# Kernel optimization log

Measured on AMD Instinct MI355X. Metric: run time of the kernel, lower is better.

Reference implementation:

```python
import jax, jax.numpy as jnp
import numpy as np

N, D, K = 65536, 256, 4096
INIT_COUNT = 100  # torch: counts = ones(K, int32) * 100


def setup_inputs() -> dict:
    key = jax.random.key(0)
    k1, k2 = jax.random.split(key)
    embedded = jax.random.normal(k1, (N, D), dtype=jnp.float32)
    centers = jax.random.normal(k2, (K, D), dtype=jnp.float32)
    counts = jnp.full((K,), INIT_COUNT, dtype=jnp.int32)
    return {"embedded": embedded, "centers": centers, "counts": counts}


def reference(embedded, centers, counts):
    # --- predict_hard: squared euclidean distance [N,K] + argmin ---
    x2 = jnp.sum(embedded * embedded, axis=1, keepdims=True)       # [N,1]
    c2 = jnp.sum(centers * centers, axis=1)                        # [K]
    d2 = x2 - 2.0 * (embedded @ centers.T) + c2                    # [N,K]
    labels = jnp.argmin(d2, axis=1).astype(jnp.int32)              # [N]

    # --- dcn_loss: mean over batch of squared dist to assigned center ---
    loss = jnp.sum((embedded - centers[labels]) ** 2) / embedded.shape[0]

    # --- update_centroids: sequential running-mean update, closed form ---
    # c <- (1-1/n)c + (1/n)x repeated over assigned samples collapses to
    # (count0 * c0 + sum_assigned x) / (count0 + m)
    seg_sum = jax.ops.segment_sum(embedded, labels, num_segments=K)            # [K,D]
    seg_cnt = jax.ops.segment_sum(
        jnp.ones((embedded.shape[0],), dtype=embedded.dtype), labels, num_segments=K
    )                                                                           # [K]
    c0 = counts.astype(embedded.dtype)                                          # [K]
    new_centers = (c0[:, None] * centers + seg_sum) / (c0 + seg_cnt)[:, None]  # [K,D]
    new_counts = counts + seg_cnt.astype(jnp.int32)                             # [K]
    return labels, new_centers, new_counts, loss
```

## Files before the change

### kernel.cpp

```cpp
#include <hip/hip_runtime.h>
#include <cfloat>
#include <cstdint>

constexpr int N  = 65536;
constexpr int D  = 256;
constexpr int K  = 4096;

typedef __attribute__((ext_vector_type(8))) _Float16 half8;
typedef __attribute__((ext_vector_type(8))) unsigned short ushort8;
typedef __attribute__((ext_vector_type(4))) float floatx4;

__device__ __forceinline__ floatx4 mfma_f16(half8 a, half8 b, floatx4 c) {
    return __builtin_amdgcn_mfma_f32_16x16x32_f16(a, b, c, 0, 0, 0);
}

__device__ __forceinline__ void ld_lds16(void* lds, const void* g) {
    __builtin_amdgcn_global_load_lds(
        (const __attribute__((address_space(1))) unsigned int*)g,
        (__attribute__((address_space(3))) unsigned int*)lds, 16, 0, 0);
}

__global__ void prep_c2(const float* __restrict__ C, float* __restrict__ c2) {
    int k = blockIdx.x;
    int l = threadIdx.x;
    const float4* row = (const float4*)(C + (size_t)k * D);
    float4 v = row[l];
    float s = v.x*v.x + v.y*v.y + v.z*v.z + v.w*v.w;
    #pragma unroll
    for (int m = 1; m < 64; m <<= 1) s += __shfl_xor(s, m);
    if (l == 0) c2[k] = s;
}

__global__ void convert_f16_both(const float* __restrict__ X, const float* __restrict__ C,
                                 unsigned short* __restrict__ Xh,
                                 unsigned short* __restrict__ Cf,
                                 float* __restrict__ xsq_part,
                                 float* __restrict__ c2) {
    __shared__ float red[4];
    int id = blockIdx.x * 256 + threadIdx.x;
    const int nX = N * D / 8;
    bool isX = id < nX;
    const float* src;
    if (isX) { src = X; }
    else     { src = C; id -= nX; }
    const float4* s4 = (const float4*)src;
    float4 a = s4[2*id], b = s4[2*id+1];
    float xs[8] = {a.x,a.y,a.z,a.w,b.x,b.y,b.z,b.w};
    ushort8 h;
    float ps = 0.f;
    #pragma unroll
    for (int i = 0; i < 8; ++i) {
        union { _Float16 f; unsigned short u; } cv;
        cv.f = (_Float16)xs[i];
        h[i] = cv.u;
        ps += xs[i]*xs[i];
    }
    int t = threadIdx.x;
    if (isX) {
        ((ushort8*)Xh)[id] = h;
        #pragma unroll
        for (int m = 1; m < 64; m <<= 1) ps += __shfl_xor(ps, m);
        if ((t & 63) == 0) red[t >> 6] = ps;
        __syncthreads();
        if (t == 0) xsq_part[blockIdx.x] = (red[0] + red[1]) + (red[2] + red[3]);
    } else {
        int c    = id >> 5;
        int dk   = (id >> 2) & 7;
        int quad = id & 3;
        int flat = (((c >> 6) * 8 + dk) * 4 + ((c >> 4) & 3)) * 64 + quad * 16 + (c & 15);
        ((ushort8*)Cf)[flat] = h;
        #pragma unroll
        for (int m = 1; m < 32; m <<= 1) ps += __shfl_xor(ps, m);
        if ((t & 31) == 0) c2[c] = ps;
    }
}

__global__ __launch_bounds__(256, 2) void mfma_assign(
        const unsigned short* __restrict__ Xh, const unsigned short* __restrict__ Cfu,
        const float* __restrict__ c2, float* __restrict__ cand)
{
    __shared__ __align__(16) unsigned short sA[8*128*4*8];

    const int t    = threadIdx.x;
    const int w    = t >> 6, l = t & 63;
    const int quad = l >> 4, lr = l & 15;
    const int wm   = w >> 1, wn = w & 1;
    const int rowbase = blockIdx.x * 128;
    const int kb   = blockIdx.y;

    const int rl  = l >> 2;
    const int gsw = (l & 3) ^ ((l >> 3) & 3);

    #pragma unroll
    for (int k = 0; k < 16; ++k) {
        int q = w*16 + k;
        int c = q >> 3, rb = (q & 7) * 16;
        const unsigned short* gp = Xh + (size_t)(rowbase + rb + rl)*D + c*32 + gsw*8;
        ld_lds16((char*)sA + q*1024, gp);
    }

    const half8* pB = (const half8*)Cfu + (size_t)(kb*16 + wn)*2048 + l;
    const char* sAc = (const char*)sA;
    const int sA_off = ((64*wm + lr)*4 + (quad ^ ((lr>>1)&3)))*16;

    half8 A0[4], A1[4], B0[4], B1[4];

#define LOADB(Bs, bump) do {                                            \
        Bs[0] = pB[0]; Bs[1] = pB[64]; Bs[2] = pB[128]; Bs[3] = pB[192]; \
        pB += (bump); } while (0)

#define LOADA(As, dkn) do {                                             \
        As[0] = *(const half8*)(sAc + ((dkn)*8192 + 0*1024) + sA_off);  \
        As[1] = *(const half8*)(sAc + ((dkn)*8192 + 1*1024) + sA_off);  \
        As[2] = *(const half8*)(sAc + ((dkn)*8192 + 2*1024) + sA_off);  \
        As[3] = *(const half8*)(sAc + ((dkn)*8192 + 3*1024) + sA_off); } while (0)

#define MF16(As, Bs) do {                                               \
        _Pragma("unroll")                                               \
        for (int j_ = 0; j_ < 4; ++j_)                                  \
            _Pragma("unroll")                                           \
            for (int i_ = 0; i_ < 4; ++i_)                              \
                acc[i_][j_] = mfma_f16(As[i_], Bs[j_], acc[i_][j_]); } while (0)

    LOADB(B0, 256);
    __syncthreads();
    LOADA(A0, 0);

    float v1[16], v2[16]; int x1[16], x2s[16];
    #pragma unroll
    for (int i = 0; i < 16; ++i) { v1[i]=FLT_MAX; v2[i]=FLT_MAX; x1[i]=0x7fffffff; x2s[i]=0x7fffffff; }

    floatx4 acc[4][4];
    float c2v[4]; int jidx[4];

    for (int e = 0; e < 8; ++e) {
        #pragma unroll
        for (int i = 0; i < 4; ++i)
            #pragma unroll
            for (int j = 0; j < 4; ++j) acc[i][j] = (floatx4)0.f;
        const int colbase = (kb*8 + e)*128 + 64*wn;
        #pragma unroll
        for (int j = 0; j < 4; ++j) {
            int col = colbase + 16*j + lr;
            c2v[j] = c2[col]; jidx[j] = col;
        }

        LOADB(B1, 256);  LOADA(A1, 1); MF16(A0, B0);
        LOADB(B0, 256);  LOADA(A0, 2); MF16(A1, B1);
        LOADB(B1, 256);  LOADA(A1, 3); MF16(A0, B0);
        LOADB(B0, 256);  LOADA(A0, 4); MF16(A1, B1);
        LOADB(B1, 256);  LOADA(A1, 5); MF16(A0, B0);
        LOADB(B0, 256);  LOADA(A0, 6); MF16(A1, B1);
        LOADB(B1, 2304); LOADA(A1, 7); MF16(A0, B0);
        LOADB(B0, 256);  LOADA(A0, 0); MF16(A1, B1);

        #pragma unroll
        for (int i = 0; i < 4; ++i)
            #pragma unroll
            for (int j = 0; j < 4; ++j)
                #pragma unroll
                for (int r = 0; r < 4; ++r) {
                    float s = fmaf(-2.f, acc[i][j][r], c2v[j]);
                    int st = 4*i + r;
                    bool cA = s < v1[st];
                    bool cB = s < v2[st];
                    float tv = cB ? s : v2[st]; int tx = cB ? jidx[j] : x2s[st];
                    v2[st] = cA ? v1[st] : tv;  x2s[st] = cA ? x1[st] : tx;
                    v1[st] = cA ? s : v1[st];   x1[st]  = cA ? jidx[j] : x1[st];
                }
    }

#undef LOADB
#undef LOADA
#undef MF16

    #pragma unroll
    for (int i = 0; i < 4; ++i)
        #pragma unroll
        for (int r = 0; r < 4; ++r) {
            int st = 4*i + r;
            float a1 = v1[st], a2 = v2[st]; int ax1 = x1[st], ax2 = x2s[st];
            #pragma unroll
            for (int m = 1; m < 16; m <<= 1) {
                float b1f = __shfl_xor(a1, m); int bx1 = __shfl_xor(ax1, m);
                float b2f = __shfl_xor(a2, m); int bx2 = __shfl_xor(ax2, m);
                bool tt = (b1f < a1) || (b1f == a1 && bx1 < ax1);
                float n1 = tt ? b1f : a1; int nx1 = tt ? bx1 : ax1;
                float w1 = tt ? a1 : b1f; int wx1 = tt ? ax1 : bx1;
                float w2 = tt ? b2f : a2; int wx2 = tt ? bx2 : ax2;
                bool uu = (w2 < w1) || (w2 == w1 && wx2 < wx1);
                a1 = n1; ax1 = nx1;
                a2 = uu ? w2 : w1; ax2 = uu ? wx2 : wx1;
            }
            if (lr == 0) {
                int row = rowbase + 64*wm + 16*i + 4*quad + r;
                float4 o; o.x = a1; o.y = __int_as_float(ax1);
                o.z = a2; o.w = __int_as_float(ax2);
                ((float4*)cand)[(size_t)row*8 + 2*kb + wn] = o;
            }
        }
}

__global__ __launch_bounds__(256) void recheck_label(
        const float* __restrict__ X, const float* __restrict__ C,
        const float* __restrict__ c2, const float* __restrict__ cand,
        float* __restrict__ out_labels, int* __restrict__ labInt,
        int* __restrict__ cnt)
{
    int t = threadIdx.x, w = t >> 6, l = t & 63;
    int g  = l >> 4;
    int lr = l & 15;
    int row0 = (blockIdx.x * 4 + w) * 4;
    int row  = row0 + g;

    float4 e = ((const float4*)cand)[(size_t)row*8 + (lr >> 1)];
    float s  = (lr & 1) ? e.z : e.x;
    int  idx = (lr & 1) ? __float_as_int(e.w) : __float_as_int(e.y);

    float a1 = s, a2 = FLT_MAX; int ax1 = idx, ax2 = 0x7fffffff;
    #pragma unroll
    for (int m = 1; m < 16; m <<= 1) {
        float b1 = __shfl_xor(a1, m); int bx1 = __shfl_xor(ax1, m);
        float b2 = __shfl_xor(a2, m); int bx2 = __shfl_xor(ax2, m);
        bool tt = (b1 < a1) || (b1 == a1 && bx1 < ax1);
        float n1 = tt ? b1 : a1; int nx1 = tt ? bx1 : ax1;
        float w1 = tt ? a1 : b1; int wx1 = tt ? ax1 : bx1;
        float w2 = tt ? b2 : a2; int wx2 = tt ? bx2 : ax2;
        bool uu = (w2 < w1) || (w2 == w1 && wx2 < wx1);
        a1 = n1; ax1 = nx1;
        a2 = uu ? w2 : w1; ax2 = uu ? wx2 : wx1;
    }

    bool certain = (a2 - a1 > 0.25f);
    unsigned long long certMask = __ballot(certain);

    if (certain && lr == 0) {
        out_labels[row] = (float)ax1;
        labInt[row] = ax1;
        atomicAdd(&cnt[ax1], 1);
    }

    #pragma unroll
    for (int q = 0; q < 4; ++q) {
        if ((certMask >> (q*16)) & 1ull) continue;
        int r = row0 + q;
        float sq  = __shfl(s,   q*16 + lr);
        int   iq  = __shfl(idx, q*16 + lr);
        float gs1 = __shfl(a1,  q*16);

        float4 xv = ((const float4*)X)[(size_t)r*64 + l];
        float px = xv.x*xv.x + xv.y*xv.y + xv.z*xv.z + xv.w*xv.w;
        #pragma unroll
        for (int m = 1; m < 64; m <<= 1) px += __shfl_xor(px, m);

        bool active = (l < 16) && (sq <= gs1 + 0.25f);
        unsigned long long mask = __ballot(active);
        float best = FLT_MAX; int bi = 0x7fffffff;
        while (mask) {
            int k = __ffsll((long long)mask) - 1;
            mask &= mask - 1;
            int ck = __shfl(iq, k);
            float4 cv = ((const float4*)C)[(size_t)ck*64 + l];
            float pd = xv.x*cv.x + xv.y*cv.y + xv.z*cv.z + xv.w*cv.w;
            #pragma unroll
            for (int m = 1; m < 64; m <<= 1) pd += __shfl_xor(pd, m);
            float d2 = fmaf(-2.f, pd, px) + c2[ck];
            if (d2 < best || (d2 == best && ck < bi)) { best = d2; bi = ck; }
        }
        if (l == 0) {
            out_labels[r] = (float)bi;
            labInt[r] = bi;
            atomicAdd(&cnt[bi], 1);
        }
    }
}

__global__ void prefix_kernel(const int* __restrict__ cnt,
                              int* __restrict__ offs, int* __restrict__ cursor) {
    int l = threadIdx.x;
    int s = 0;
    #pragma unroll 8
    for (int i = 0; i < 64; ++i) s += cnt[l*64 + i];
    int inc = s;
    #pragma unroll
    for (int off = 1; off < 64; off <<= 1) {
        int u = __shfl_up(inc, off);
        if (l >= off) inc += u;
    }
    int run = inc - s;
    for (int i = 0; i < 64; ++i) {
        int k = l*64 + i;
        offs[k] = run; cursor[k] = run;
        run += cnt[k];
    }
}

__global__ void scatter_idx(const int* __restrict__ labInt,
                            int* __restrict__ cursor, int* __restrict__ sortedIdx) {
    int i = blockIdx.x * 256 + threadIdx.x;
    int lab = labInt[i];
    int pos = atomicAdd(&cursor[lab], 1);
    sortedIdx[pos] = i;
}

__global__ __launch_bounds__(256) void center_update(
        const float* __restrict__ X, const float* __restrict__ C,
        const int* __restrict__ counts0, const int* __restrict__ cnt,
        const int* __restrict__ offs, const int* __restrict__ sortedIdx,
        float* __restrict__ lossC, float* __restrict__ out)
{
    __shared__ float red[4];
    int k = blockIdx.x, d = threadIdx.x;
    int start = offs[k], m = cnt[k];
    float acc = 0.f;
    int i = 0;
    for (; i + 4 <= m; i += 4) {
        int r0 = sortedIdx[start+i],   r1 = sortedIdx[start+i+1];
        int r2 = sortedIdx[start+i+2], r3 = sortedIdx[start+i+3];
        float a0 = X[(size_t)r0*D + d], a1 = X[(size_t)r1*D + d];
        float a2 = X[(size_t)r2*D + d], a3 = X[(size_t)r3*D + d];
        acc += (a0 + a1) + (a2 + a3);
    }
    for (; i < m; ++i) acc += X[(size_t)sortedIdx[start+i]*D + d];

    float cv = C[(size_t)k*D + d];
    float c0 = (float)counts0[k];
    out[N + (size_t)k*D + d] = (c0 * cv + acc) / (c0 + (float)m);
    if (d == 0) out[N + (size_t)K*D + k] = (float)(counts0[k] + m);

    float lp = cv * fmaf((float)m, cv, -2.f*acc);
    #pragma unroll
    for (int s = 1; s < 64; s <<= 1) lp += __shfl_xor(lp, s);
    if ((d & 63) == 0) red[d >> 6] = lp;
    __syncthreads();
    if (d == 0) lossC[k] = (red[0] + red[1]) + (red[2] + red[3]);
}

__global__ __launch_bounds__(256) void loss_final(
        const float* __restrict__ xsq_part, const float* __restrict__ lossC,
        float* __restrict__ out)
{
    __shared__ double red[4];
    int t = threadIdx.x;
    double s = 0.0;
    for (int i = t; i < 8192; i += 256) s += (double)xsq_part[i];
    for (int i = t; i < 4096; i += 256) s += (double)lossC[i];
    #pragma unroll
    for (int m = 1; m < 64; m <<= 1) s += __shfl_xor(s, m);
    if ((t & 63) == 0) red[t >> 6] = s;
    __syncthreads();
    if (t == 0)
        out[N + (size_t)K*D + K] = (float)(((red[0] + red[1]) + (red[2] + red[3])) / (double)N);
}

__global__ void finalize_kernel(const float* __restrict__ C,
                                const int* __restrict__ counts0,
                                const float* __restrict__ seg,
                                const int* __restrict__ cnt,
                                const double* __restrict__ lossAcc,
                                float* __restrict__ out)
{
    int g = blockIdx.x * 256 + threadIdx.x;
    int k = g >> 8;
    float c0 = (float)counts0[k];
    float m  = (float)cnt[k];
    out[N + g] = (c0 * C[g] + seg[g]) / (c0 + m);
    if (g < K) out[N + (size_t)K*D + g] = (float)(counts0[g] + cnt[g]);
    if (g == 0) out[N + (size_t)K*D + K] = (float)(lossAcc[0] / (double)N);
}

__global__ __launch_bounds__(256, 2) void assign_fp32(
        const float* __restrict__ X, const float* __restrict__ C,
        const float* __restrict__ c2, float* __restrict__ out_labels,
        float* __restrict__ seg, int* __restrict__ cnt,
        double* __restrict__ lossAcc)
{
    constexpr int BM = 128, BN = 128, KD = 16;
    __shared__ float As[KD][BM];
    __shared__ float Bs[KD][BN];
    __shared__ float x2f[BM];
    __shared__ int   labs[BM];

    const int t  = threadIdx.x;
    const int tx = t & 15;
    const int ty = t >> 4;
    const int rowbase = blockIdx.x * BM;

    {
        int r  = t >> 1;
        int dh = (t & 1) * (D / 2);
        const float4* xr = (const float4*)(X + (size_t)(rowbase + r) * D + dh);
        float s = 0.f;
        #pragma unroll
        for (int i = 0; i < D / 8; ++i) {
            float4 v = xr[i];
            s += v.x*v.x + v.y*v.y + v.z*v.z + v.w*v.w;
        }
        s += __shfl_xor(s, 1);
        if ((t & 1) == 0) x2f[r] = s;
    }
    __syncthreads();

    float x2v[8];
    #pragma unroll
    for (int i = 0; i < 4; ++i) { x2v[i] = x2f[4*ty + i]; x2v[i+4] = x2f[64 + 4*ty + i]; }

    float rmv[8]; int rmi[8];
    #pragma unroll
    for (int i = 0; i < 8; ++i) { rmv[i] = FLT_MAX; rmi[i] = 0x7fffffff; }

    for (int ct = 0; ct < K / BN; ++ct) {
        float acc[8][8];
        #pragma unroll
        for (int i = 0; i < 8; ++i)
            #pragma unroll
            for (int j = 0; j < 8; ++j) acc[i][j] = 0.f;

        float c2f2[8];
        {
            float4 a = *(const float4*)(c2 + ct*BN + 4*tx);
            float4 b = *(const float4*)(c2 + ct*BN + 64 + 4*tx);
            c2f2[0]=a.x; c2f2[1]=a.y; c2f2[2]=a.z; c2f2[3]=a.w;
            c2f2[4]=b.x; c2f2[5]=b.y; c2f2[6]=b.z; c2f2[7]=b.w;
        }

        for (int dk = 0; dk < D / KD; ++dk) {
            #pragma unroll
            for (int i = 0; i < 2; ++i) {
                int f  = t + 256 * i;
                int r  = f >> 2;
                int dp = f & 3;
                float4 av = *(const float4*)(X + (size_t)(rowbase + r) * D + dk*KD + 4*dp);
                float4 bv = *(const float4*)(C + (size_t)(ct*BN + r) * D + dk*KD + 4*dp);
                As[4*dp+0][r]=av.x; As[4*dp+1][r]=av.y; As[4*dp+2][r]=av.z; As[4*dp+3][r]=av.w;
                Bs[4*dp+0][r]=bv.x; Bs[4*dp+1][r]=bv.y; Bs[4*dp+2][r]=bv.z; Bs[4*dp+3][r]=bv.w;
            }
            __syncthreads();
            #pragma unroll
            for (int kk = 0; kk < KD; ++kk) {
                float4 a0 = *(const float4*)&As[kk][4*ty];
                float4 a1 = *(const float4*)&As[kk][64 + 4*ty];
                float4 b0 = *(const float4*)&Bs[kk][4*tx];
                float4 b1 = *(const float4*)&Bs[kk][64 + 4*tx];
                float av[8] = {a0.x,a0.y,a0.z,a0.w,a1.x,a1.y,a1.z,a1.w};
                float bv[8] = {b0.x,b0.y,b0.z,b0.w,b1.x,b1.y,b1.z,b1.w};
                #pragma unroll
                for (int i = 0; i < 8; ++i)
                    #pragma unroll
                    for (int j = 0; j < 8; ++j)
                        acc[i][j] = fmaf(av[i], bv[j], acc[i][j]);
            }
            __syncthreads();
        }

        #pragma unroll
        for (int i = 0; i < 8; ++i) {
            float bv = FLT_MAX; int bi = 0x7fffffff;
            #pragma unroll
            for (int j = 0; j < 8; ++j) {
                int coll = (j < 4) ? (4*tx + j) : (64 + 4*tx + (j - 4));
                float v = fmaf(-2.f, acc[i][j], x2v[i]) + c2f2[j];
                int idx = ct * BN + coll;
                if (v < bv || (v == bv && idx < bi)) { bv = v; bi = idx; }
            }
            #pragma unroll
            for (int m = 1; m < 16; m <<= 1) {
                float ov = __shfl_xor(bv, m);
                int   oi = __shfl_xor(bi, m);
                if (ov < bv || (ov == bv && oi < bi)) { bv = ov; bi = oi; }
            }
            if (bv < rmv[i] || (bv == rmv[i] && bi < rmi[i])) { rmv[i] = bv; rmi[i] = bi; }
        }
    }

    if (tx == 0) {
        #pragma unroll
        for (int i = 0; i < 8; ++i) {
            int r = (i < 4) ? (4*ty + i) : (64 + 4*ty + (i - 4));
            labs[r] = rmi[i];
            out_labels[rowbase + r] = (float)rmi[i];
            atomicAdd(&cnt[rmi[i]], 1);
        }
    }
    __syncthreads();

    {
        int r   = t >> 1;
        int dh  = (t & 1) * (D / 2);
        int lab = labs[r];
        const float4* xr = (const float4*)(X + (size_t)(rowbase + r) * D + dh);
        const float4* cr = (const float4*)(C + (size_t)lab * D + dh);
        float* sp = seg + (size_t)lab * D + dh;
        float ls = 0.f;
        #pragma unroll 8
        for (int i = 0; i < D / 8; ++i) {
            float4 xv = xr[i];
            float4 cv = cr[i];
            atomicAdd(sp + 4*i + 0, xv.x);
            atomicAdd(sp + 4*i + 1, xv.y);
            atomicAdd(sp + 4*i + 2, xv.z);
            atomicAdd(sp + 4*i + 3, xv.w);
            float d0 = xv.x - cv.x, d1 = xv.y - cv.y;
            float d2 = xv.z - cv.z, d3 = xv.w - cv.w;
            ls += d0*d0 + d1*d1 + d2*d2 + d3*d3;
        }
        #pragma unroll
        for (int m = 1; m < 64; m <<= 1) ls += __shfl_xor(ls, m);
        if ((t & 63) == 0) atomicAdd(lossAcc, (double)ls);
    }
}

extern "C" void kernel_launch(void* const* d_in, const int* in_sizes, int n_in,
                              void* d_out, int out_size, void* d_ws, size_t ws_size,
                              hipStream_t stream) {
    const float* X       = (const float*)d_in[0];
    const float* C       = (const float*)d_in[1];
    const int*   counts0 = (const int*)d_in[2];
    float* out = (float*)d_out;

    char* p = (char*)d_ws;
    float*  seg     = (float*)p;          p += (size_t)K * D * 4;
    int*    cnt     = (int*)p;            p += (size_t)K * 4;
    float*  c2      = (float*)p;          p += (size_t)K * 4;
    double* lossAcc = (double*)p;         p += 16;
    size_t zero_all = (size_t)(p - (char*)d_ws);
    float*  cand    = (float*)p;          p += (size_t)N * 32 * 4;
    unsigned short* Xh = (unsigned short*)p; p += (size_t)N * D * 2;
    unsigned short* Cf = (unsigned short*)p; p += (size_t)K * D * 2;
    float* xsq_part = (float*)p;          p += 8192 * 4;
    float* lossC    = (float*)p;          p += (size_t)K * 4;
    size_t need = (size_t)(p - (char*)d_ws);

    int* labInt    = (int*)seg;
    int* sortedIdx = labInt + N;
    int* offs      = sortedIdx + N;
    int* cursor    = offs + K;

    if (ws_size >= need) {
        hipMemsetAsync(cnt, 0, (size_t)K * 4, stream);
        convert_f16_both<<<(N*D/8 + K*D/8)/256, 256, 0, stream>>>(X, C, Xh, Cf, xsq_part, c2);
        mfma_assign<<<dim3(N/128, 4), 256, 0, stream>>>(Xh, Cf, c2, cand);
        recheck_label<<<N/16, 256, 0, stream>>>(X, C, c2, cand, out, labInt, cnt);
        prefix_kernel<<<1, 64, 0, stream>>>(cnt, offs, cursor);
        scatter_idx<<<N/256, 256, 0, stream>>>(labInt, cursor, sortedIdx);
        center_update<<<K, 256, 0, stream>>>(X, C, counts0, cnt, offs, sortedIdx, lossC, out);
        loss_final<<<1, 256, 0, stream>>>(xsq_part, lossC, out);
    } else {
        hipMemsetAsync(d_ws, 0, zero_all, stream);
        prep_c2<<<K, 64, 0, stream>>>(C, c2);
        assign_fp32<<<N/128, 256, 0, stream>>>(X, C, c2, out, seg, cnt, lossAcc);
        finalize_kernel<<<(K*D)/256, 256, 0, stream>>>(C, counts0, seg, cnt, lossAcc, out);
    }
}
```

Measured before the change: 626.4 us.

## Repartition MFMA assign kernel so each wave owns 32 rows across all columns

Changes the wave tiling in the fp16 MFMA distance/argmin kernel from a 2x2 arrangement (64 rows x 64 cols per wave) to four waves each owning 32 rows and sweeping every column tile of the block's K slice. Per-wave accumulator and top-2 state registers are halved, and the A fragments now come straight from LDS each step instead of being double-buffered. Candidates are flushed once per half of the K slice so the output layout stays the same. In exchange, each wave streams twice as much B data from global memory per row, and the MFMA work per B load drops.

```diff
diff --git a/kernel.cpp b/kernel.cpp
--- a/kernel.cpp
+++ b/kernel.cpp
@@ -84,7 +84,6 @@
     const int t    = threadIdx.x;
     const int w    = t >> 6, l = t & 63;
     const int quad = l >> 4, lr = l & 15;
-    const int wm   = w >> 1, wn = w & 1;
     const int rowbase = blockIdx.x * 128;
     const int kb   = blockIdx.y;
 
@@ -99,106 +98,106 @@
         ld_lds16((char*)sA + q*1024, gp);
     }
 
-    const half8* pB = (const half8*)Cfu + (size_t)(kb*16 + wn)*2048 + l;
+    const half8* pB = (const half8*)Cfu + (size_t)kb*32768 + l;
     const char* sAc = (const char*)sA;
-    const int sA_off = ((64*wm + lr)*4 + (quad ^ ((lr>>1)&3)))*16;
-
-    half8 A0[4], A1[4], B0[4], B1[4];
-
-#define LOADB(Bs, bump) do {                                            \
+    const int sA_off = ((32*w + lr)*4 + (quad ^ ((lr>>1)&3)))*16;
+
+    half8 B0[4], B1[4];
+    floatx4 acc[2][4];
+    float c2v[4]; int jidx[4];
+    float v1[8], v2[8]; int x1[8], x2s[8];
+
+#define LOADB(Bs) do {                                                   \
         Bs[0] = pB[0]; Bs[1] = pB[64]; Bs[2] = pB[128]; Bs[3] = pB[192]; \
-        pB += (bump); } while (0)
-
-#define LOADA(As, dkn) do {                                             \
-        As[0] = *(const half8*)(sAc + ((dkn)*8192 + 0*1024) + sA_off);  \
-        As[1] = *(const half8*)(sAc + ((dkn)*8192 + 1*1024) + sA_off);  \
-        As[2] = *(const half8*)(sAc + ((dkn)*8192 + 2*1024) + sA_off);  \
-        As[3] = *(const half8*)(sAc + ((dkn)*8192 + 3*1024) + sA_off); } while (0)
-
-#define MF16(As, Bs) do {                                               \
-        _Pragma("unroll")                                               \
-        for (int j_ = 0; j_ < 4; ++j_)                                  \
-            _Pragma("unroll")                                           \
-            for (int i_ = 0; i_ < 4; ++i_)                              \
-                acc[i_][j_] = mfma_f16(As[i_], Bs[j_], acc[i_][j_]); } while (0)
-
-    LOADB(B0, 256);
+        pB += 256; } while (0)
+
+#define STEP(dk, Bc) do {                                                \
+        half8 Af0 = *(const half8*)(sAc + (dk)*8192 + 0*1024 + sA_off);  \
+        half8 Af1 = *(const half8*)(sAc + (dk)*8192 + 1*1024 + sA_off);  \
+        _Pragma("unroll")                                                \
+        for (int j_ = 0; j_ < 4; ++j_) {                                 \
+            acc[0][j_] = mfma_f16(Af0, Bc[j_], acc[0][j_]);              \
+            acc[1][j_] = mfma_f16(Af1, Bc[j_], acc[1][j_]);              \
+        } } while (0)
+
+#define FLUSH(h) do {                                                       \
+    _Pragma("unroll")                                                       \
+    for (int i = 0; i < 2; ++i)                                             \
+        _Pragma("unroll")                                                   \
+        for (int r = 0; r < 4; ++r) {                                       \
+            int st = 4*i + r;                                               \
+            float a1 = v1[st], a2 = v2[st]; int ax1 = x1[st], ax2 = x2s[st];\
+            _Pragma("unroll")                                               \
+            for (int m = 1; m < 16; m <<= 1) {                              \
+                float b1f = __shfl_xor(a1, m); int bx1 = __shfl_xor(ax1, m);\
+                float b2f = __shfl_xor(a2, m); int bx2 = __shfl_xor(ax2, m);\
+                bool tt = (b1f < a1) || (b1f == a1 && bx1 < ax1);           \
+                float n1 = tt ? b1f : a1; int nx1 = tt ? bx1 : ax1;         \
+                float w1 = tt ? a1 : b1f; int wx1 = tt ? ax1 : bx1;         \
+                float w2 = tt ? b2f : a2; int wx2 = tt ? bx2 : ax2;         \
+                bool uu = (w2 < w1) || (w2 == w1 && wx2 < wx1);             \
+                a1 = n1; ax1 = nx1;                                         \
+                a2 = uu ? w2 : w1; ax2 = uu ? wx2 : wx1;                    \
+            }                                                               \
+            if (lr == 0) {                                                  \
+                int row = rowbase + 32*w + 16*i + 4*quad + r;               \
+                float4 o; o.x = a1; o.y = __int_as_float(ax1);              \
+                o.z = a2; o.w = __int_as_float(ax2);                        \
+                ((float4*)cand)[(size_t)row*8 + (h)] = o;                   \
+            }                                                               \
+            v1[st] = FLT_MAX; v2[st] = FLT_MAX;                             \
+            x1[st] = 0x7fffffff; x2s[st] = 0x7fffffff;                      \
+        } } while (0)
+
+    LOADB(B0);
     __syncthreads();
-    LOADA(A0, 0);
-
-    float v1[16], v2[16]; int x1[16], x2s[16];
-    #pragma unroll
-    for (int i = 0; i < 16; ++i) { v1[i]=FLT_MAX; v2[i]=FLT_MAX; x1[i]=0x7fffffff; x2s[i]=0x7fffffff; }
-
-    floatx4 acc[4][4];
-    float c2v[4]; int jidx[4];
-
-    for (int e = 0; e < 8; ++e) {
-        #pragma unroll
-        for (int i = 0; i < 4; ++i)
-            #pragma unroll
-            for (int j = 0; j < 4; ++j) acc[i][j] = (floatx4)0.f;
-        const int colbase = (kb*8 + e)*128 + 64*wn;
-        #pragma unroll
-        for (int j = 0; j < 4; ++j) {
-            int col = colbase + 16*j + lr;
-            c2v[j] = c2[col]; jidx[j] = col;
-        }
-
-        LOADB(B1, 256);  LOADA(A1, 1); MF16(A0, B0);
-        LOADB(B0, 256);  LOADA(A0, 2); MF16(A1, B1);
-        LOADB(B1, 256);  LOADA(A1, 3); MF16(A0, B0);
-        LOADB(B0, 256);  LOADA(A0, 4); MF16(A1, B1);
-        LOADB(B1, 256);  LOADA(A1, 5); MF16(A0, B0);
-        LOADB(B0, 256);  LOADA(A0, 6); MF16(A1, B1);
-        LOADB(B1, 2304); LOADA(A1, 7); MF16(A0, B0);
-        LOADB(B0, 256);  LOADA(A0, 0); MF16(A1, B1);
-
-        #pragma unroll
-        for (int i = 0; i < 4; ++i)
-            #pragma unroll
-            for (int j = 0; j < 4; ++j)
+
+    #pragma unroll
+    for (int i = 0; i < 8; ++i) { v1[i]=FLT_MAX; v2[i]=FLT_MAX; x1[i]=0x7fffffff; x2s[i]=0x7fffffff; }
+
+    for (int half = 0; half < 2; ++half) {
+        for (int e8 = 0; e8 < 8; ++e8) {
+            const int ct64 = kb*16 + half*8 + e8;
+            #pragma unroll
+            for (int i = 0; i < 2; ++i)
                 #pragma unroll
-                for (int r = 0; r < 4; ++r) {
-                    float s = fmaf(-2.f, acc[i][j][r], c2v[j]);
-                    int st = 4*i + r;
-                    bool cA = s < v1[st];
-                    bool cB = s < v2[st];
-                    float tv = cB ? s : v2[st]; int tx = cB ? jidx[j] : x2s[st];
-                    v2[st] = cA ? v1[st] : tv;  x2s[st] = cA ? x1[st] : tx;
-                    v1[st] = cA ? s : v1[st];   x1[st]  = cA ? jidx[j] : x1[st];
-                }
+                for (int j = 0; j < 4; ++j) acc[i][j] = (floatx4)0.f;
+            #pragma unroll
+            for (int j = 0; j < 4; ++j) {
+                int col = ct64*64 + 16*j + lr;
+                c2v[j] = c2[col]; jidx[j] = col;
+            }
+
+            LOADB(B1); STEP(0, B0);
+            LOADB(B0); STEP(1, B1);
+            LOADB(B1); STEP(2, B0);
+            LOADB(B0); STEP(3, B1);
+            LOADB(B1); STEP(4, B0);
+            LOADB(B0); STEP(5, B1);
+            LOADB(B1); STEP(6, B0);
+            LOADB(B0); STEP(7, B1);
+
+            #pragma unroll
+            for (int i = 0; i < 2; ++i)
+                #pragma unroll
+                for (int j = 0; j < 4; ++j)
+                    #pragma unroll
+                    for (int r = 0; r < 4; ++r) {
+                        float s = fmaf(-2.f, acc[i][j][r], c2v[j]);
+                        int st = 4*i + r;
+                        bool cA = s < v1[st];
+                        bool cB = s < v2[st];
+                        float tv = cB ? s : v2[st]; int tx = cB ? jidx[j] : x2s[st];
+                        v2[st] = cA ? v1[st] : tv;  x2s[st] = cA ? x1[st] : tx;
+                        v1[st] = cA ? s : v1[st];   x1[st]  = cA ? jidx[j] : x1[st];
+                    }
+        }
+        FLUSH(2*kb + half);
     }
 
 #undef LOADB
-#undef LOADA
-#undef MF16
-
-    #pragma unroll
-    for (int i = 0; i < 4; ++i)
-        #pragma unroll
-        for (int r = 0; r < 4; ++r) {
-            int st = 4*i + r;
-            float a1 = v1[st], a2 = v2[st]; int ax1 = x1[st], ax2 = x2s[st];
-            #pragma unroll
-            for (int m = 1; m < 16; m <<= 1) {
-                float b1f = __shfl_xor(a1, m); int bx1 = __shfl_xor(ax1, m);
-                float b2f = __shfl_xor(a2, m); int bx2 = __shfl_xor(ax2, m);
-                bool tt = (b1f < a1) || (b1f == a1 && bx1 < ax1);
-                float n1 = tt ? b1f : a1; int nx1 = tt ? bx1 : ax1;
-                float w1 = tt ? a1 : b1f; int wx1 = tt ? ax1 : bx1;
-                float w2 = tt ? b2f : a2; int wx2 = tt ? bx2 : ax2;
-                bool uu = (w2 < w1) || (w2 == w1 && wx2 < wx1);
-                a1 = n1; ax1 = nx1;
-                a2 = uu ? w2 : w1; ax2 = uu ? wx2 : wx1;
-            }
-            if (lr == 0) {
-                int row = rowbase + 64*wm + 16*i + 4*quad + r;
-                float4 o; o.x = a1; o.y = __int_as_float(ax1);
-                o.z = a2; o.w = __int_as_float(ax2);
-                ((float4*)cand)[(size_t)row*8 + 2*kb + wn] = o;
-            }
-        }
+#undef STEP
+#undef FLUSH
 }
 
 __global__ __launch_bounds__(256) void recheck_label(
```

After: 657.4 us. +4.9%, slower.
